# Performance work log

Measured on AMD Instinct MI355X. Metric: run time of the kernel, lower is better.

Reference implementation:

```python
import jax, jax.numpy as jnp
import numpy as np

B, N, D = 4, 2048, 1024
H = 16
HD = D // H  # head_dim = 64
SCALE = HD ** -0.5


def setup_inputs() -> dict:
    key = jax.random.key(0)
    k1, k2, k3, k4 = jax.random.split(key, 4)
    x = jax.random.normal(k1, (B, N, D), dtype=jnp.float32)
    # init-scale weights for numerically sane softmax logits
    w_qkv = jax.random.normal(k2, (3 * D, D), dtype=jnp.float32) * 0.02
    w_proj = jax.random.normal(k3, (D, D), dtype=jnp.float32) * 0.02
    b_proj = jax.random.normal(k4, (D,), dtype=jnp.float32) * 0.02
    return {"x": x, "w_qkv": w_qkv, "w_proj": w_proj, "b_proj": b_proj}


def reference(x, w_qkv, w_proj, b_proj):
    # qkv projection (width_mult=1.0 -> Dyna slicing is identity; qkv_bias=False)
    qkv = jnp.einsum('bnd,ed->bne', x, w_qkv)          # (B, N, 3D)
    qkv = qkv.reshape(B, N, 3, H, HD)
    q = qkv[:, :, 0].transpose(0, 2, 1, 3)              # (B, H, N, HD)
    k = qkv[:, :, 1].transpose(0, 2, 1, 3)
    v = qkv[:, :, 2].transpose(0, 2, 1, 3)
    q = q * SCALE
    attn = jnp.einsum('bhqd,bhkd->bhqk', q, k)          # (B, H, N, N)
    attn = jax.nn.softmax(attn, axis=-1)
    out = jnp.einsum('bhqk,bhkd->bhqd', attn, v)        # (B, H, N, HD)
    out = out.transpose(0, 2, 1, 3).reshape(B, N, D)
    # output projection (bias=True)
    return jnp.einsum('bnd,ed->bne', out, w_proj) + b_proj
```

## Files before the change

kernel.cpp:

```cpp
#include <hip/hip_runtime.h>
#include <hip/hip_bf16.h>
#include <stdint.h>


typedef __attribute__((ext_vector_type(8))) short short8;
typedef __attribute__((ext_vector_type(4))) short short4v;
typedef __attribute__((ext_vector_type(4))) float float4v;
typedef __attribute__((ext_vector_type(16))) float float16v;

#define MFMA16(a, b, c) __builtin_amdgcn_mfma_f32_16x16x32_bf16((a), (b), (c), 0, 0, 0)
#define MFMA32(a, b, c) __builtin_amdgcn_mfma_f32_32x32x16_bf16((a), (b), (c), 0, 0, 0)

static __device__ __forceinline__ unsigned short f2bf(float f) {
  union { float f; unsigned u; } v; v.f = f;
  unsigned r = v.u + 0x7fffu + ((v.u >> 16) & 1u);
  return (unsigned short)(r >> 16);
}
static __device__ __forceinline__ float bf2f(unsigned short u) {
  union { unsigned u; float f; } v; v.u = ((unsigned)u) << 16;
  return v.f;
}
static __device__ __forceinline__ unsigned pkbf(float a, float b) {
  union { __hip_bfloat162 v; unsigned u; } c;
  c.v = __float22bfloat162_rn(make_float2(a, b));
  return c.u;
}
static __device__ __forceinline__ float ex2(float x) {
#if __has_builtin(__builtin_amdgcn_exp2f)
  return __builtin_amdgcn_exp2f(x);
#else
  return exp2f(x);
#endif
}
static __device__ __forceinline__ float4v fzero() {
  float4v z; z[0] = 0.f; z[1] = 0.f; z[2] = 0.f; z[3] = 0.f; return z;
}
static __device__ __forceinline__ float16v fzero16() {
  float16v z;
#pragma unroll
  for (int i = 0; i < 16; ++i) z[i] = 0.f;
  return z;
}
static __device__ __forceinline__ void pl32swap(unsigned& a, unsigned& b) {
  asm volatile("v_permlane32_swap_b32 %0, %1" : "+v"(a), "+v"(b));
}
static __device__ __forceinline__ void load_lds16(const void* g, void* l) {
  typedef const __attribute__((address_space(1))) void* gp_t;
  typedef __attribute__((address_space(3))) void* lp_t;
  __builtin_amdgcn_global_load_lds((gp_t)(uintptr_t)g, (lp_t)(uint32_t)(uintptr_t)l, 16, 0, 0);
}

__global__ void detect_dtype(const unsigned short* __restrict__ x, int* flag) {
  __shared__ int cnt;
  if (threadIdx.x == 0) cnt = 0;
  __syncthreads();
  int c = 0;
  for (int i = threadIdx.x; i < 4096; i += 256) {
    const unsigned v = x[i] & 0x7FFFu;
    if ((v >> 7) >= 134u) ++c;
  }
  atomicAdd(&cnt, c);
  __syncthreads();
  if (threadIdx.x == 0) *flag = (cnt > 64) ? 1 : 0;
}

static __device__ __forceinline__ void cv8(const void* src, unsigned short* dst,
                                           int i, int fl) {
  if (fl) {
    const float4v a = *(const float4v*)((const float*)src + i);
    const float4v b = *(const float4v*)((const float*)src + i + 4);
    short8 o;
    o[0] = (short)f2bf(a[0]); o[1] = (short)f2bf(a[1]);
    o[2] = (short)f2bf(a[2]); o[3] = (short)f2bf(a[3]);
    o[4] = (short)f2bf(b[0]); o[5] = (short)f2bf(b[1]);
    o[6] = (short)f2bf(b[2]); o[7] = (short)f2bf(b[3]);
    *(short8*)(dst + i) = o;
  } else {
    *(short8*)(dst + i) = *(const short8*)((const unsigned short*)src + i);
  }
}
__global__ __launch_bounds__(256) void convert_all(
    const void* __restrict__ s0, const void* __restrict__ s1,
    const void* __restrict__ s2, const void* __restrict__ s3,
    unsigned short* __restrict__ d0, unsigned short* __restrict__ d1,
    unsigned short* __restrict__ d2, unsigned short* __restrict__ d3,
    const int* __restrict__ flag) {
  const int t = blockIdx.x * 256 + threadIdx.x;
  const int fl = *flag;
  if (t < 1048576)       cv8(s0, d0, t * 8, fl);
  else if (t < 1441792)  cv8(s1, d1, (t - 1048576) * 8, fl);
  else if (t < 1572864)  cv8(s2, d2, (t - 1441792) * 8, fl);
  else if (t < 1572992)  cv8(s3, d3, (t - 1572864) * 8, fl);
}

__global__ __launch_bounds__(256) void qkv_gemm(
    const unsigned short* __restrict__ X, const unsigned short* __restrict__ W,
    unsigned short* __restrict__ Qo, unsigned short* __restrict__ Ko,
    unsigned short* __restrict__ Vt) {
  __shared__ __attribute__((aligned(16))) unsigned short lA[2][128 * 32];
  __shared__ __attribute__((aligned(16))) unsigned short lB[2][128 * 32];
  const int tid = threadIdx.x;
  const int wave = tid >> 6, lane = tid & 63, quad = lane >> 4, l16 = lane & 15;
  const int wm = wave >> 1, wn = wave & 1;
  const int m0 = blockIdx.x * 128, n0 = blockIdx.y * 128;

  float4v acc[4][4];
  for (int i = 0; i < 4; ++i) for (int j = 0; j < 4; ++j) acc[i][j] = fzero();

  const int f0 = tid, f1 = 256 + tid;
  const int r0 = f0 >> 2, c0 = (f0 & 3) * 8;
  const int r1 = f1 >> 2, c1 = (f1 & 3) * 8;
  const int dof0 = (wave * 64) * 8;
  const int dof1 = (256 + wave * 64) * 8;

#define QKV_STAGE(buf, k0)                                                   \
  load_lds16(X + (size_t)(m0 + r0) * 1024 + (k0) + c0, lA[buf] + dof0);      \
  load_lds16(X + (size_t)(m0 + r1) * 1024 + (k0) + c1, lA[buf] + dof1);      \
  load_lds16(W + (size_t)(n0 + r0) * 1024 + (k0) + c0, lB[buf] + dof0);      \
  load_lds16(W + (size_t)(n0 + r1) * 1024 + (k0) + c1, lB[buf] + dof1);

  QKV_STAGE(0, 0);
  __syncthreads();
  int cur = 0;
  for (int k0 = 0; k0 < 1024; k0 += 32) {
    if (k0 < 992) { QKV_STAGE(cur ^ 1, k0 + 32); }
    short8 af[4], bfr[4];
    for (int t = 0; t < 4; ++t) {
      af[t]  = *(const short8*)(lA[cur] + (wm * 64 + t * 16 + l16) * 32 + quad * 8);
      bfr[t] = *(const short8*)(lB[cur] + (wn * 64 + t * 16 + l16) * 32 + quad * 8);
    }
    for (int mt = 0; mt < 4; ++mt)
      for (int nt = 0; nt < 4; ++nt)
        acc[mt][nt] = MFMA16(af[mt], bfr[nt], acc[mt][nt]);
    __syncthreads();
    cur ^= 1;
  }
#undef QKV_STAGE

  const float QSCALE = 0.18033688011112042f;
  for (int mt = 0; mt < 4; ++mt) {
    const int mbase = m0 + wm * 64 + mt * 16 + quad * 4;
    const int b = mbase >> 11;
    const int nrow = mbase & 2047;
    for (int nt = 0; nt < 4; ++nt) {
      const int e = n0 + wn * 64 + nt * 16 + l16;
      const int c = e >> 10, h = (e >> 6) & 15, hd = e & 63;
      const int bh = b * 16 + h;
      if (c == 0) {
        for (int r = 0; r < 4; ++r)
          Qo[((size_t)bh * 2048 + nrow + r) * 64 + hd] = f2bf(acc[mt][nt][r] * QSCALE);
      } else if (c == 1) {
        for (int r = 0; r < 4; ++r)
          Ko[((size_t)bh * 2048 + nrow + r) * 64 + hd] = f2bf(acc[mt][nt][r]);
      } else {
        short4v pk;
        for (int r = 0; r < 4; ++r) pk[r] = (short)f2bf(acc[mt][nt][r]);
        *(short4v*)(Vt + ((size_t)bh * 64 + hd) * 2048 + nrow) = pk;
      }
    }
  }
}

__global__ __launch_bounds__(256, 4) void flash_attn(
    const unsigned short* __restrict__ Q, const unsigned short* __restrict__ K,
    const unsigned short* __restrict__ Vt, unsigned short* __restrict__ AO) {
  __shared__ __attribute__((aligned(16))) unsigned short lK[2][64 * 72];
  __shared__ __attribute__((aligned(16))) unsigned short lV[2][64 * 72];
  const int tid = threadIdx.x;
  const int wave = tid >> 6, lane = tid & 63;
  const int l31 = lane & 31, hi = lane >> 5;
  const int qt = blockIdx.x, bh = blockIdx.y;
  const int b = bh >> 4, h = bh & 15;
  const size_t base = (size_t)bh * 2048 * 64;
  const unsigned short* Qp = Q + base;
  const unsigned short* Kp = K + base;
  const unsigned short* Vp = Vt + base;
  const int q0 = qt * 128;

  const int qa = q0 + wave * 32 + l31;
  short8 qf[4];
#pragma unroll
  for (int j = 0; j < 4; ++j)
    qf[j] = *(const short8*)(Qp + (size_t)qa * 64 + j * 16 + hi * 8);

  float16v oacc0 = fzero16(), oacc1 = fzero16();
  float lsum = 0.f;

  const int f0 = tid, f1 = 256 + tid;
  const int sk0 = (f0 >> 3) * 72 + (f0 & 7) * 8;
  const int sk1 = (f1 >> 3) * 72 + (f1 & 7) * 8;

  short8 kv0 = *(const short8*)(Kp + f0 * 8);
  short8 kv1 = *(const short8*)(Kp + f1 * 8);
  short8 vv0 = *(const short8*)(Vp + (size_t)(f0 >> 3) * 2048 + (f0 & 7) * 8);
  short8 vv1 = *(const short8*)(Vp + (size_t)(f1 >> 3) * 2048 + (f1 & 7) * 8);

  for (int kb = 0; kb < 32; ++kb) {
    unsigned short* const Kb = lK[kb & 1];
    unsigned short* const Vb = lV[kb & 1];
    *(short8*)(Kb + sk0) = kv0;
    *(short8*)(Kb + sk1) = kv1;
    *(short8*)(Vb + sk0) = vv0;
    *(short8*)(Vb + sk1) = vv1;
    __syncthreads();
    if (kb < 31) {
      const size_t ko = (size_t)(kb + 1) * 4096;
      kv0 = *(const short8*)(Kp + ko + f0 * 8);
      kv1 = *(const short8*)(Kp + ko + f1 * 8);
      vv0 = *(const short8*)(Vp + (size_t)(f0 >> 3) * 2048 + (kb + 1) * 64 + (f0 & 7) * 8);
      vv1 = *(const short8*)(Vp + (size_t)(f1 >> 3) * 2048 + (kb + 1) * 64 + (f1 & 7) * 8);
    }

#pragma unroll
    for (int kb2 = 0; kb2 < 2; ++kb2) {
      const unsigned short* krow = Kb + (kb2 * 32 + l31) * 72 + hi * 8;
      float16v s = fzero16();
#pragma unroll
      for (int j = 0; j < 4; ++j)
        s = MFMA32(*(const short8*)(krow + j * 16), qf[j], s);

      unsigned u[8];
      float ls = 0.f;
#pragma unroll
      for (int j = 0; j < 8; ++j) {
        const float e0 = ex2(s[2 * j]);
        const float e1 = ex2(s[2 * j + 1]);
        ls += e0 + e1;
        u[j] = pkbf(e0, e1);
      }
      lsum += ls;

      pl32swap(u[0], u[2]); pl32swap(u[1], u[3]);
      pl32swap(u[4], u[6]); pl32swap(u[5], u[7]);
      union { unsigned w[4]; short8 s8; } fr0, fr1;
      fr0.w[0] = u[0]; fr0.w[1] = u[1]; fr0.w[2] = u[2]; fr0.w[3] = u[3];
      fr1.w[0] = u[4]; fr1.w[1] = u[5]; fr1.w[2] = u[6]; fr1.w[3] = u[7];

      const unsigned short* vrow0 = Vb + l31 * 72 + kb2 * 32 + hi * 8;
      const unsigned short* vrow1 = vrow0 + 32 * 72;
      oacc0 = MFMA32(*(const short8*)(vrow0), fr0.s8, oacc0);
      oacc1 = MFMA32(*(const short8*)(vrow1), fr0.s8, oacc1);
      oacc0 = MFMA32(*(const short8*)(vrow0 + 16), fr1.s8, oacc0);
      oacc1 = MFMA32(*(const short8*)(vrow1 + 16), fr1.s8, oacc1);
    }
  }

  lsum += __shfl_xor(lsum, 32);
  const float inv = 1.f / lsum;

  unsigned short* ao = AO + ((size_t)(b * 2048 + qa)) * 1024 + h * 64 + hi * 4;
#pragma unroll
  for (int mt = 0; mt < 2; ++mt) {
    const float16v& oc = mt ? oacc1 : oacc0;
#pragma unroll
    for (int g = 0; g < 4; ++g) {
      union { unsigned u2[2]; short4v s4; } o;
      o.u2[0] = pkbf(oc[4 * g] * inv, oc[4 * g + 1] * inv);
      o.u2[1] = pkbf(oc[4 * g + 2] * inv, oc[4 * g + 3] * inv);
      *(short4v*)(ao + mt * 32 + g * 8) = o.s4;
    }
  }
}

__global__ __launch_bounds__(256) void proj_gemm(
    const unsigned short* __restrict__ A, const unsigned short* __restrict__ W,
    const unsigned short* __restrict__ bias_bf, const void* __restrict__ bias_raw,
    void* __restrict__ outv, const int* __restrict__ flag) {
  __shared__ __attribute__((aligned(16))) unsigned short lA[2][128 * 32];
  __shared__ __attribute__((aligned(16))) unsigned short lB[2][128 * 32];
  const int tid = threadIdx.x;
  const int wave = tid >> 6, lane = tid & 63, quad = lane >> 4, l16 = lane & 15;
  const int wm = wave >> 1, wn = wave & 1;
  const int m0 = blockIdx.x * 128, n0 = blockIdx.y * 128;
  const int fl = *flag;

  float4v acc[4][4];
  for (int i = 0; i < 4; ++i) for (int j = 0; j < 4; ++j) acc[i][j] = fzero();

  const int f0 = tid, f1 = 256 + tid;
  const int r0 = f0 >> 2, c0 = (f0 & 3) * 8;
  const int r1 = f1 >> 2, c1 = (f1 & 3) * 8;
  const int dof0 = (wave * 64) * 8;
  const int dof1 = (256 + wave * 64) * 8;

#define PROJ_STAGE(buf, k0)                                                  \
  load_lds16(A + (size_t)(m0 + r0) * 1024 + (k0) + c0, lA[buf] + dof0);      \
  load_lds16(A + (size_t)(m0 + r1) * 1024 + (k0) + c1, lA[buf] + dof1);     \
  load_lds16(W + (size_t)(n0 + r0) * 1024 + (k0) + c0, lB[buf] + dof0);      \
  load_lds16(W + (size_t)(n0 + r1) * 1024 + (k0) + c1, lB[buf] + dof1);

  PROJ_STAGE(0, 0);
  __syncthreads();
  int cur = 0;
  for (int k0 = 0; k0 < 1024; k0 += 32) {
    if (k0 < 992) { PROJ_STAGE(cur ^ 1, k0 + 32); }
    short8 af[4], bfr[4];
    for (int t = 0; t < 4; ++t) {
      af[t]  = *(const short8*)(lA[cur] + (wm * 64 + t * 16 + l16) * 32 + quad * 8);
      bfr[t] = *(const short8*)(lB[cur] + (wn * 64 + t * 16 + l16) * 32 + quad * 8);
    }
    for (int mt = 0; mt < 4; ++mt)
      for (int nt = 0; nt < 4; ++nt)
        acc[mt][nt] = MFMA16(af[mt], bfr[nt], acc[mt][nt]);
    __syncthreads();
    cur ^= 1;
  }
#undef PROJ_STAGE

  for (int mt = 0; mt < 4; ++mt) {
    const int mbase = m0 + wm * 64 + mt * 16 + quad * 4;
    for (int nt = 0; nt < 4; ++nt) {
      const int e = n0 + wn * 64 + nt * 16 + l16;
      const float bv = fl ? ((const float*)bias_raw)[e] : bf2f(bias_bf[e]);
      for (int r = 0; r < 4; ++r) {
        const float val = acc[mt][nt][r] + bv;
        const size_t idx = (size_t)(mbase + r) * 1024 + e;
        if (fl) ((float*)outv)[idx] = val;
        else    ((unsigned short*)outv)[idx] = f2bf(val);
      }
    }
  }
}

extern "C" void kernel_launch(void* const* d_in, const int* in_sizes, int n_in,
                              void* d_out, int out_size, void* d_ws, size_t ws_size,
                              hipStream_t stream) {
  const void* x_raw     = d_in[0];
  const void* wqkv_raw  = d_in[1];
  const void* wproj_raw = d_in[2];
  const void* bproj_raw = d_in[3];

  const size_t NE = (size_t)4 * 16 * 2048 * 64;
  unsigned short* ws = (unsigned short*)d_ws;
  unsigned short* Q      = ws;
  unsigned short* K      = Q + NE;
  unsigned short* Vt     = K + NE;
  unsigned short* xb     = Vt + NE;
  unsigned short* AO     = xb;
  unsigned short* wqkvb  = xb + NE;
  unsigned short* wprojb = wqkvb + 3145728;
  unsigned short* bprojb = wprojb + 1048576;
  int* flag = (int*)(bprojb + 1024);

  detect_dtype<<<1, 256, 0, stream>>>((const unsigned short*)x_raw, flag);
  convert_all<<<6145, 256, 0, stream>>>(x_raw, wqkv_raw, wproj_raw, bproj_raw,
                                        xb, wqkvb, wprojb, bprojb, flag);

  qkv_gemm<<<dim3(64, 24), 256, 0, stream>>>(xb, wqkvb, Q, K, Vt);
  flash_attn<<<dim3(16, 64), 256, 0, stream>>>(Q, K, Vt, AO);
  proj_gemm<<<dim3(64, 8), 256, 0, stream>>>(AO, wprojb, bprojb, bproj_raw,
                                             d_out, flag);
}
```

Baseline: 279.1 us.

## Deepen GEMM LDS pipeline to four buffers with one barrier per k-step

The QKV and output-projection GEMMs move from a double-buffered LDS ring to a 4-slot ring with a prefetch distance of two k-tiles. Explicit vmcnt waits stand in for __syncthreads, leaving a single barrier per iteration. The goal is to keep more global-to-LDS loads in flight and cut barrier stalls. In exchange, LDS use per block doubles to 64KB, which may reduce occupancy, and correctness relies on the manual vmcnt counting.

```diff
diff --git a/kernel.cpp b/kernel.cpp
--- a/kernel.cpp
+++ b/kernel.cpp
@@ -97,8 +97,8 @@
     const unsigned short* __restrict__ X, const unsigned short* __restrict__ W,
     unsigned short* __restrict__ Qo, unsigned short* __restrict__ Ko,
     unsigned short* __restrict__ Vt) {
-  __shared__ __attribute__((aligned(16))) unsigned short lA[2][128 * 32];
-  __shared__ __attribute__((aligned(16))) unsigned short lB[2][128 * 32];
+  __shared__ __attribute__((aligned(16))) unsigned short lA[4][128 * 32];
+  __shared__ __attribute__((aligned(16))) unsigned short lB[4][128 * 32];
   const int tid = threadIdx.x;
   const int wave = tid >> 6, lane = tid & 63, quad = lane >> 4, l16 = lane & 15;
   const int wm = wave >> 1, wn = wave & 1;
@@ -119,23 +119,36 @@
   load_lds16(W + (size_t)(n0 + r0) * 1024 + (k0) + c0, lB[buf] + dof0);      \
   load_lds16(W + (size_t)(n0 + r1) * 1024 + (k0) + c1, lB[buf] + dof1);
 
+#define QKV_COMPUTE(kk)                                                      \
+  {                                                                          \
+    const unsigned short* sA = lA[(kk) & 3];                                 \
+    const unsigned short* sB = lB[(kk) & 3];                                 \
+    short8 af[4], bfr[4];                                                    \
+    for (int t = 0; t < 4; ++t) {                                            \
+      af[t]  = *(const short8*)(sA + (wm * 64 + t * 16 + l16) * 32 + quad * 8); \
+      bfr[t] = *(const short8*)(sB + (wn * 64 + t * 16 + l16) * 32 + quad * 8); \
+    }                                                                        \
+    for (int mt = 0; mt < 4; ++mt)                                           \
+      for (int nt = 0; nt < 4; ++nt)                                         \
+        acc[mt][nt] = MFMA16(af[mt], bfr[nt], acc[mt][nt]);                  \
+  }
+
   QKV_STAGE(0, 0);
-  __syncthreads();
-  int cur = 0;
-  for (int k0 = 0; k0 < 1024; k0 += 32) {
-    if (k0 < 992) { QKV_STAGE(cur ^ 1, k0 + 32); }
-    short8 af[4], bfr[4];
-    for (int t = 0; t < 4; ++t) {
-      af[t]  = *(const short8*)(lA[cur] + (wm * 64 + t * 16 + l16) * 32 + quad * 8);
-      bfr[t] = *(const short8*)(lB[cur] + (wn * 64 + t * 16 + l16) * 32 + quad * 8);
-    }
-    for (int mt = 0; mt < 4; ++mt)
-      for (int nt = 0; nt < 4; ++nt)
-        acc[mt][nt] = MFMA16(af[mt], bfr[nt], acc[mt][nt]);
-    __syncthreads();
-    cur ^= 1;
-  }
+  QKV_STAGE(1, 32);
+  for (int k = 0; k < 30; ++k) {
+    QKV_STAGE((k + 2) & 3, k * 32 + 64);
+    asm volatile("s_waitcnt vmcnt(8)" ::: "memory");
+    __builtin_amdgcn_s_barrier();
+    QKV_COMPUTE(k);
+  }
+  asm volatile("s_waitcnt vmcnt(4)" ::: "memory");
+  __builtin_amdgcn_s_barrier();
+  QKV_COMPUTE(30);
+  asm volatile("s_waitcnt vmcnt(0)" ::: "memory");
+  __builtin_amdgcn_s_barrier();
+  QKV_COMPUTE(31);
 #undef QKV_STAGE
+#undef QKV_COMPUTE
 
   const float QSCALE = 0.18033688011112042f;
   for (int mt = 0; mt < 4; ++mt) {
@@ -266,8 +279,8 @@
     const unsigned short* __restrict__ A, const unsigned short* __restrict__ W,
     const unsigned short* __restrict__ bias_bf, const void* __restrict__ bias_raw,
     void* __restrict__ outv, const int* __restrict__ flag) {
-  __shared__ __attribute__((aligned(16))) unsigned short lA[2][128 * 32];
-  __shared__ __attribute__((aligned(16))) unsigned short lB[2][128 * 32];
+  __shared__ __attribute__((aligned(16))) unsigned short lA[4][128 * 32];
+  __shared__ __attribute__((aligned(16))) unsigned short lB[4][128 * 32];
   const int tid = threadIdx.x;
   const int wave = tid >> 6, lane = tid & 63, quad = lane >> 4, l16 = lane & 15;
   const int wm = wave >> 1, wn = wave & 1;
@@ -285,27 +298,40 @@
 
 #define PROJ_STAGE(buf, k0)                                                  \
   load_lds16(A + (size_t)(m0 + r0) * 1024 + (k0) + c0, lA[buf] + dof0);      \
-  load_lds16(A + (size_t)(m0 + r1) * 1024 + (k0) + c1, lA[buf] + dof1);     \
+  load_lds16(A + (size_t)(m0 + r1) * 1024 + (k0) + c1, lA[buf] + dof1);      \
   load_lds16(W + (size_t)(n0 + r0) * 1024 + (k0) + c0, lB[buf] + dof0);      \
   load_lds16(W + (size_t)(n0 + r1) * 1024 + (k0) + c1, lB[buf] + dof1);
 
+#define PROJ_COMPUTE(kk)                                                     \
+  {                                                                          \
+    const unsigned short* sA = lA[(kk) & 3];                                 \
+    const unsigned short* sB = lB[(kk) & 3];                                 \
+    short8 af[4], bfr[4];                                                    \
+    for (int t = 0; t < 4; ++t) {                                            \
+      af[t]  = *(const short8*)(sA + (wm * 64 + t * 16 + l16) * 32 + quad * 8); \
+      bfr[t] = *(const short8*)(sB + (wn * 64 + t * 16 + l16) * 32 + quad * 8); \
+    }                                                                        \
+    for (int mt = 0; mt < 4; ++mt)                                           \
+      for (int nt = 0; nt < 4; ++nt)                                         \
+        acc[mt][nt] = MFMA16(af[mt], bfr[nt], acc[mt][nt]);                  \
+  }
+
   PROJ_STAGE(0, 0);
-  __syncthreads();
-  int cur = 0;
-  for (int k0 = 0; k0 < 1024; k0 += 32) {
-    if (k0 < 992) { PROJ_STAGE(cur ^ 1, k0 + 32); }
-    short8 af[4], bfr[4];
-    for (int t = 0; t < 4; ++t) {
-      af[t]  = *(const short8*)(lA[cur] + (wm * 64 + t * 16 + l16) * 32 + quad * 8);
-      bfr[t] = *(const short8*)(lB[cur] + (wn * 64 + t * 16 + l16) * 32 + quad * 8);
-    }
-    for (int mt = 0; mt < 4; ++mt)
-      for (int nt = 0; nt < 4; ++nt)
-        acc[mt][nt] = MFMA16(af[mt], bfr[nt], acc[mt][nt]);
-    __syncthreads();
-    cur ^= 1;
-  }
+  PROJ_STAGE(1, 32);
+  for (int k = 0; k < 30; ++k) {
+    PROJ_STAGE((k + 2) & 3, k * 32 + 64);
+    asm volatile("s_waitcnt vmcnt(8)" ::: "memory");
+    __builtin_amdgcn_s_barrier();
+    PROJ_COMPUTE(k);
+  }
+  asm volatile("s_waitcnt vmcnt(4)" ::: "memory");
+  __builtin_amdgcn_s_barrier();
+  PROJ_COMPUTE(30);
+  asm volatile("s_waitcnt vmcnt(0)" ::: "memory");
+  __builtin_amdgcn_s_barrier();
+  PROJ_COMPUTE(31);
 #undef PROJ_STAGE
+#undef PROJ_COMPUTE
 
   for (int mt = 0; mt < 4; ++mt) {
     const int mbase = m0 + wm * 64 + mt * 16 + quad * 4;
```

Result: no change. 282.0 us (+1.0%).

## Double QKV GEMM K-tile to 64 and XOR-swizzle LDS layout

Applied to the files above, without the earlier changes.

The QKV projection GEMM now stages 64-wide K slices per iteration instead of 32, which halves the number of barrier-separated iterations. The LDS layout uses an XOR swizzle on 16-byte chunks so that fragment reads hit fewer bank conflicts. The cost is twice the LDS per block (64 KB), which may lower occupancy, plus some extra index arithmetic.

```diff
diff --git a/kernel.cpp b/kernel.cpp
--- a/kernel.cpp
+++ b/kernel.cpp
@@ -97,8 +97,8 @@
     const unsigned short* __restrict__ X, const unsigned short* __restrict__ W,
     unsigned short* __restrict__ Qo, unsigned short* __restrict__ Ko,
     unsigned short* __restrict__ Vt) {
-  __shared__ __attribute__((aligned(16))) unsigned short lA[2][128 * 32];
-  __shared__ __attribute__((aligned(16))) unsigned short lB[2][128 * 32];
+  __shared__ __attribute__((aligned(16))) unsigned short lA[2][128 * 64];
+  __shared__ __attribute__((aligned(16))) unsigned short lB[2][128 * 64];
   const int tid = threadIdx.x;
   const int wave = tid >> 6, lane = tid & 63, quad = lane >> 4, l16 = lane & 15;
   const int wm = wave >> 1, wn = wave & 1;
@@ -107,31 +107,49 @@
   float4v acc[4][4];
   for (int i = 0; i < 4; ++i) for (int j = 0; j < 4; ++j) acc[i][j] = fzero();
 
-  const int f0 = tid, f1 = 256 + tid;
-  const int r0 = f0 >> 2, c0 = (f0 & 3) * 8;
-  const int r1 = f1 >> 2, c1 = (f1 & 3) * 8;
-  const int dof0 = (wave * 64) * 8;
-  const int dof1 = (256 + wave * 64) * 8;
-
-#define QKV_STAGE(buf, k0)                                                   \
-  load_lds16(X + (size_t)(m0 + r0) * 1024 + (k0) + c0, lA[buf] + dof0);      \
-  load_lds16(X + (size_t)(m0 + r1) * 1024 + (k0) + c1, lA[buf] + dof1);      \
-  load_lds16(W + (size_t)(n0 + r0) * 1024 + (k0) + c0, lB[buf] + dof0);      \
-  load_lds16(W + (size_t)(n0 + r1) * 1024 + (k0) + c1, lB[buf] + dof1);
+  int srow[4], scol[4];
+#pragma unroll
+  for (int r = 0; r < 4; ++r) {
+    const int f = r * 256 + tid;
+    srow[r] = f >> 3;
+    scol[r] = ((f & 7) ^ (srow[r] & 7)) * 8;
+  }
+  const int lsw = l16 & 7;
+
+#define QKV_STAGE(buf, k0)                                                    \
+  {                                                                           \
+    _Pragma("unroll")                                                         \
+    for (int r = 0; r < 4; ++r) {                                             \
+      const int dof = (r * 256 + wave * 64) * 8;                              \
+      load_lds16(X + (size_t)(m0 + srow[r]) * 1024 + (k0) + scol[r],          \
+                 lA[buf] + dof);                                              \
+      load_lds16(W + (size_t)(n0 + srow[r]) * 1024 + (k0) + scol[r],          \
+                 lB[buf] + dof);                                              \
+    }                                                                         \
+  }
 
   QKV_STAGE(0, 0);
   __syncthreads();
   int cur = 0;
-  for (int k0 = 0; k0 < 1024; k0 += 32) {
-    if (k0 < 992) { QKV_STAGE(cur ^ 1, k0 + 32); }
-    short8 af[4], bfr[4];
-    for (int t = 0; t < 4; ++t) {
-      af[t]  = *(const short8*)(lA[cur] + (wm * 64 + t * 16 + l16) * 32 + quad * 8);
-      bfr[t] = *(const short8*)(lB[cur] + (wn * 64 + t * 16 + l16) * 32 + quad * 8);
-    }
-    for (int mt = 0; mt < 4; ++mt)
-      for (int nt = 0; nt < 4; ++nt)
-        acc[mt][nt] = MFMA16(af[mt], bfr[nt], acc[mt][nt]);
+  for (int k0 = 0; k0 < 1024; k0 += 64) {
+    if (k0 < 960) { QKV_STAGE(cur ^ 1, k0 + 64); }
+#pragma unroll
+    for (int ks = 0; ks < 2; ++ks) {
+      short8 af[4], bfr[4];
+#pragma unroll
+      for (int t = 0; t < 4; ++t) {
+        const int rowA = wm * 64 + t * 16 + l16;
+        const int rowB = wn * 64 + t * 16 + l16;
+        const int ch = ((ks * 4 + quad) ^ lsw) * 8;
+        af[t]  = *(const short8*)(lA[cur] + rowA * 64 + ch);
+        bfr[t] = *(const short8*)(lB[cur] + rowB * 64 + ch);
+      }
+#pragma unroll
+      for (int mt = 0; mt < 4; ++mt)
+#pragma unroll
+        for (int nt = 0; nt < 4; ++nt)
+          acc[mt][nt] = MFMA16(af[mt], bfr[nt], acc[mt][nt]);
+    }
     __syncthreads();
     cur ^= 1;
   }
```

Result: faster. 261.3 us (-6.4%).
